# Kernel optimization log

Measured on AMD Instinct MI355X. Metric: run time of the kernel, lower is better.

## Reference

```python
import jax, jax.numpy as jnp
import numpy as np

WS = 3          # windows_size
ND = 3          # num_dilation, dilations [1,2,3]
NSTATE = 16     # d_state
RANK = 12       # dt_rank = ceil(192/16)
TOPK = 36       # max(1,(20//3)**2)*depth
DM = 192        # d_model
DI = 384        # d_inner = 2*d_model
B0, HH, WW = 8, 96, 96


def setup_inputs() -> dict:
    ks = jax.random.split(jax.random.key(0), 12)
    f = jax.random.normal
    return {
        "x": f(ks[0], (B0, HH, WW, DM), jnp.float32),
        "W_in": f(ks[1], (2 * DI, DM), jnp.float32) * 0.02,
        "conv_w": f(ks[2], (DI, 1, 7, 7), jnp.float32) * 0.05,
        "conv_b": f(ks[3], (DI,), jnp.float32) * 0.01,
        "x_proj_w": f(ks[4], (2, RANK + 2 * NSTATE, DI), jnp.float32) * 0.02,
        "dt_w": f(ks[5], (2, DI, RANK), jnp.float32) * 0.02,
        "dt_b": f(ks[6], (2, DI), jnp.float32) * 0.01,
        "A_logs": jnp.tile(jnp.log(jnp.arange(1, NSTATE + 1, dtype=jnp.float32)), (2 * DI, 1)),
        "Ds": jnp.ones((2 * DI,), jnp.float32),
        "W_kv": f(ks[7], (2 * DI, DI), jnp.float32) * 0.02,
        "b_kv": jnp.zeros((2 * DI,), jnp.float32),
        "ln_g": jnp.ones((DI,), jnp.float32),
        "ln_b": jnp.zeros((DI,), jnp.float32),
        "W_out": f(ks[8], (DM, DI), jnp.float32) * 0.02,
    }


def _selective_scan(xs, x_proj_w, dt_w, dt_b, A_logs, Ds):
    # xs: (B, K=2, D, L) -> (B, K, D, L). Standard Mamba selective scan.
    B, K, D, L = xs.shape
    x_dbl = jnp.einsum('bkdl,kcd->bkcl', xs, x_proj_w)          # (B,K,R+2N,L)
    dts = x_dbl[:, :, :RANK]
    Bs = x_dbl[:, :, RANK:RANK + NSTATE]                        # (B,K,N,L)
    Cs = x_dbl[:, :, RANK + NSTATE:]                            # (B,K,N,L)
    delta = jax.nn.softplus(jnp.einsum('bkrl,kdr->bkdl', dts, dt_w) + dt_b[None, :, :, None])
    A = -jnp.exp(A_logs).reshape(K, D, NSTATE)
    dA = jnp.exp(delta[..., None] * A[None, :, :, None, :])    # (B,K,D,L,N)
    dBu = delta[..., None] * Bs.transpose(0, 1, 3, 2)[:, :, None, :, :] * xs[..., None]
    dA = jnp.moveaxis(dA, 3, 0)                                 # (L,B,K,D,N)
    dBu = jnp.moveaxis(dBu, 3, 0)
    C = jnp.moveaxis(Cs, 3, 0)                                  # (L,B,K,N)

    def step(h, inp):
        dA_t, dBu_t, C_t = inp
        h = dA_t * h + dBu_t
        y = jnp.einsum('bkdn,bkn->bkd', h, C_t)
        return h, y

    h0 = jnp.zeros((B, K, D, NSTATE), xs.dtype)
    _, ys = jax.lax.scan(step, h0, (dA, dBu, C))                # ys: (L,B,K,D)
    y = jnp.moveaxis(ys, 0, 3)                                  # (B,K,D,L)
    return y + Ds.reshape(1, K, D, 1) * xs


def _dynamic_mask_active(x):
    # x: (B,D,H,W). Partition into WSxWS windows, keep TOPK by mean activation.
    B, D, H, W = x.shape
    nH, nW = H // WS, W // WS
    w = x.reshape(B, D, nH, WS, nW, WS).transpose(0, 2, 4, 1, 3, 5)
    w = w.reshape(B, nH * nW, D, WS * WS)                       # (B,nWin,D,ws2)
    score = w.mean(axis=(2, 3))                                 # (B,nWin)
    _, idx = jax.lax.top_k(score, TOPK)                         # (B,TOPK)
    g = jnp.take_along_axis(w, idx[:, :, None, None], axis=1)   # (B,TOPK,D,ws2)
    return g.transpose(0, 2, 1, 3).reshape(B, D, TOPK * WS * WS)


def _unfold(x, d):
    # torch nn.Unfold(kernel=WS, dilation=d, padding=d, stride=1) on (B,C,H,W)
    B, C, H, W = x.shape
    xp = jnp.pad(x, ((0, 0), (0, 0), (d, d), (d, d)))
    pats = [xp[:, :, i * d:i * d + H, j * d:j * d + W] for i in range(WS) for j in range(WS)]
    p = jnp.stack(pats, axis=2)                                 # (B,C,ws2,H,W) channel-major like torch
    return p.reshape(B, C, WS * WS, H * W)


def _forward(x, W_in, conv_w, conv_b, x_proj_w, dt_w, dt_b, A_logs, Ds,
             W_kv, b_kv, ln_g, ln_b, W_out):
    B, H, W_, _ = x.shape
    xz = jnp.einsum('bhwc,oc->bhwo', x, W_in)
    xf, z = jnp.split(xz, 2, axis=-1)                           # (B,H,W,DI) each
    xc = xf.transpose(0, 3, 1, 2)
    xc = jax.lax.conv_general_dilated(xc, conv_w, (1, 1), [(3, 3), (3, 3)],
                                      feature_group_count=conv_w.shape[0],
                                      dimension_numbers=('NCHW', 'OIHW', 'NCHW'))
    xc = xc + conv_b[None, :, None, None]                       # (B,DI,H,W)
    D = xc.shape[1]

    # foreground SSM on active windows (forward + flipped scan)
    act = _dynamic_mask_active(xc)                              # (B,D,L)
    xs = jnp.stack([act, jnp.flip(act, axis=-1)], axis=1)       # (B,2,D,L)
    out = _selective_scan(xs, x_proj_w, dt_w, dt_b, A_logs, Ds)
    y1 = out[:, 0] + jnp.flip(out[:, 1], axis=-1)               # (B,D,L)
    y1 = y1.transpose(0, 2, 1)                                  # (B,L,D)

    L = y1.shape[1]
    ws2 = WS * WS
    n2 = L // ws2
    kv = jnp.einsum('bld,od->blo', y1, W_kv) + b_kv             # (B,L,2D)
    hd = 2 * D // ND
    t = kv.reshape(B, n2, ws2, ND, hd).transpose(3, 0, 4, 2, 1)  # (ND,B,hd,ws2,n2)
    Q, Kt = t[:, :, :hd // 2], t[:, :, hd // 2:]                 # (ND,B,D/ND,ws2,n2)

    dch = D // ND
    xr = xc.reshape(B, ND, dch, H, W_)
    ys = []
    for i in range(ND):
        V = _unfold(xr[:, i], i + 1)                            # (B,dch,ws2,n1)
        V = V.transpose(0, 1, 3, 2)                             # (B,dch,n1,ws2)
        s = jnp.einsum('bcwn,bcwn->bcw', Q[i], Kt[i]) / np.sqrt(dch).astype(np.float32)
        # softmax over a singleton axis (as in the source) -> all ones
        A_M = jax.nn.softmax(s[..., None], axis=-1)[..., 0]     # (B,dch,ws2)
        ys.append(jnp.einsum('bcnw,bcw->bcn', V, A_M))          # (B,dch,n1)
    y = jnp.concatenate(ys, axis=1)                             # (B,D,n1)
    y = y.transpose(0, 2, 1)                                    # (B,n1,D)

    mu = y.mean(-1, keepdims=True)
    var = y.var(-1, keepdims=True)
    y = (y - mu) / jnp.sqrt(var + 1e-5) * ln_g + ln_b
    y = y.reshape(B, H, W_, D) + z
    return jnp.einsum('bhwd,od->bhwo', y, W_out)


def reference(x, W_in, conv_w, conv_b, x_proj_w, dt_w, dt_b, A_logs, Ds,
              W_kv, b_kv, ln_g, ln_b, W_out):
    return _forward(x, W_in, conv_w, conv_b, x_proj_w, dt_w, dt_b, A_logs, Ds,
                    W_kv, b_kv, ln_g, ln_b, W_out)
```

## Files before the change

kernel.cpp:

```cpp
#include <hip/hip_runtime.h>
#include <cstddef>

#define B0V 8
#define HSV 96
#define WSV 96
#define DMV 192
#define DIV 384
#define MTOT (B0V*HSV*WSV)

typedef __attribute__((ext_vector_type(8))) unsigned short ushort8v;
typedef __attribute__((ext_vector_type(8))) short short8v;
typedef __attribute__((ext_vector_type(4))) float f32x4;
typedef _Float16 h2 __attribute__((ext_vector_type(2)));
typedef _Float16 h8 __attribute__((ext_vector_type(8)));

__device__ __forceinline__ unsigned short f2bf(float f) {
    unsigned int i; __builtin_memcpy(&i, &f, 4);
    i += 0x7FFFu + ((i >> 16) & 1);
    return (unsigned short)(i >> 16);
}

template<int ROWS>
__device__ __forceinline__ void stageBF16(const unsigned short* __restrict__ src, int ld,
                                          unsigned short* lds, int t) {
#pragma unroll
    for (int i = 0; i < ROWS*8/256; ++i) {
        const int cid = t + i*256;
        const int r = cid >> 3, cb = cid & 7;
        ushort8v sv = *(const ushort8v*)(src + (size_t)r*ld + cb*8);
        *(ushort8v*)((char*)lds + r*128 + ((cb ^ (r&7))<<4)) = sv;
    }
}
__device__ __forceinline__ short8v fragRead(const unsigned short* lds, int row, int kchunk) {
    return *(const short8v*)((const char*)lds + row*128 + ((kchunk ^ (row&7))<<4));
}

__global__ __launch_bounds__(256) void prep_kernel(
    const float* __restrict__ Wout, const float* __restrict__ Win,
    const float* __restrict__ cw,
    unsigned short* __restrict__ Wch, h2* __restrict__ w2h,
    unsigned short* __restrict__ WinfH, unsigned short* __restrict__ WoutH)
{
    const int blk = blockIdx.x;
    const int t = threadIdx.x;
    if (blk < 192) {
        __shared__ float wrow[384];
        for (int j = t; j < 384; j += 256) wrow[j] = Wout[(size_t)blk*384 + j];
        __syncthreads();
        if (t < 192) {
            float acc = 0.f;
#pragma unroll 4
            for (int j = 0; j < 384; ++j)
                acc += wrow[j] * Win[(size_t)(384 + j)*192 + t];
            Wch[(size_t)blk*192 + t] = f2bf(acc);
        }
    } else if (blk < 229) {
        const int idx = (blk - 192)*256 + t;
        if (idx < 49*192) {
            const int tap = idx / 192, cp = idx % 192;
            h2 v;
            v[0] = (_Float16)cw[(size_t)(2*cp  )*49 + tap];
            v[1] = (_Float16)cw[(size_t)(2*cp+1)*49 + tap];
            w2h[idx] = v;
        }
    } else if (blk < 265) {
        const int i = (blk - 229)*256 + t;
        if (i < 384*192/8) {
            const float4 f0 = *(const float4*)(Win + (size_t)i*8);
            const float4 f1 = *(const float4*)(Win + (size_t)i*8 + 4);
            ushort8v v;
            v[0]=f2bf(f0.x); v[1]=f2bf(f0.y); v[2]=f2bf(f0.z); v[3]=f2bf(f0.w);
            v[4]=f2bf(f1.x); v[5]=f2bf(f1.y); v[6]=f2bf(f1.z); v[7]=f2bf(f1.w);
            *(ushort8v*)(WinfH + (size_t)i*8) = v;
        }
    } else {
        const int i = (blk - 265)*256 + t;
        if (i < 192*384/8) {
            const float4 f0 = *(const float4*)(Wout + (size_t)i*8);
            const float4 f1 = *(const float4*)(Wout + (size_t)i*8 + 4);
            ushort8v v;
            v[0]=f2bf(f0.x); v[1]=f2bf(f0.y); v[2]=f2bf(f0.z); v[3]=f2bf(f0.w);
            v[4]=f2bf(f1.x); v[5]=f2bf(f1.y); v[6]=f2bf(f1.z); v[7]=f2bf(f1.w);
            *(ushort8v*)(WoutH + (size_t)i*8) = v;
        }
    }
}

__global__ __launch_bounds__(256) void gemm_in_mfma(
    const float* __restrict__ x, const unsigned short* __restrict__ Wh,
    unsigned short* __restrict__ xh, _Float16* __restrict__ xf)
{
    __shared__ unsigned short As[3*64*64];
    __shared__ unsigned short Bs[128*64];
    const int t = threadIdx.x;
    const int m0 = blockIdx.x * 64;
    const int wid = t >> 6, lane = t & 63;
    const int li = lane & 15, lg = lane >> 4;

#pragma unroll
    for (int kb = 0; kb < 3; ++kb) {
#pragma unroll
        for (int i = 0; i < 2; ++i) {
            const int cid = t + i*256;
            const int r = cid >> 3, cb = cid & 7;
            const float* p = x + (size_t)(m0 + r)*DMV + kb*64 + cb*8;
            float4 f0 = *(const float4*)p;
            float4 f1 = *(const float4*)(p+4);
            ushort8v sv;
            sv[0]=f2bf(f0.x); sv[1]=f2bf(f0.y); sv[2]=f2bf(f0.z); sv[3]=f2bf(f0.w);
            sv[4]=f2bf(f1.x); sv[5]=f2bf(f1.y); sv[6]=f2bf(f1.z); sv[7]=f2bf(f1.w);
            *(ushort8v*)((char*)(As + kb*64*64) + r*128 + ((cb ^ (r&7))<<4)) = sv;
            *(ushort8v*)(xh + (size_t)(m0 + r)*DMV + kb*64 + cb*8) = sv;
        }
    }

    for (int n0i = 0; n0i < 3; ++n0i) {
        const int n0 = n0i * 128;
        f32x4 acc[4][2];
#pragma unroll
        for (int i = 0; i < 4; ++i)
#pragma unroll
            for (int j = 0; j < 2; ++j) acc[i][j] = (f32x4){0.f,0.f,0.f,0.f};

        for (int kb = 0; kb < 3; ++kb) {
            __syncthreads();
            stageBF16<128>(Wh + (size_t)n0*DMV + kb*64, DMV, Bs, t);
            __syncthreads();
#pragma unroll
            for (int ks = 0; ks < 2; ++ks) {
                short8v a[4], b[2];
#pragma unroll
                for (int mf = 0; mf < 4; ++mf)
                    a[mf] = fragRead(As + kb*64*64, mf*16 + li, ks*4 + lg);
#pragma unroll
                for (int nf = 0; nf < 2; ++nf)
                    b[nf] = fragRead(Bs, wid*32 + nf*16 + li, ks*4 + lg);
#pragma unroll
                for (int mf = 0; mf < 4; ++mf)
#pragma unroll
                    for (int nf = 0; nf < 2; ++nf)
                        acc[mf][nf] = __builtin_amdgcn_mfma_f32_16x16x32_bf16(a[mf], b[nf], acc[mf][nf], 0, 0, 0);
            }
        }
#pragma unroll
        for (int mf = 0; mf < 4; ++mf)
#pragma unroll
            for (int nf = 0; nf < 2; ++nf)
#pragma unroll
                for (int i = 0; i < 4; ++i) {
                    const int row = m0 + mf*16 + lg*4 + i;
                    const int col = n0 + wid*32 + nf*16 + li;
                    xf[(size_t)row*DIV + col] = (_Float16)acc[mf][nf][i];
                }
    }
}

__global__ __launch_bounds__(256) void dwconv_kernel(
    const _Float16* __restrict__ xf, const h2* __restrict__ w2h,
    const float* __restrict__ cb, _Float16* __restrict__ xc)
{
    const int id  = blockIdx.x;
    const int swz = (id & 7) * 432 + (id >> 3);
    const int b    = swz / 432;
    const int rem  = swz - b*432;
    const int cg   = rem / 72;
    const int tile = rem - cg*72;
    const int th = tile / 6, tw = tile % 6;
    const int h0 = th*8, w0 = tw*16;
    const int c0 = cg*64;

    __shared__ _Float16 patch[14*22*64];
    const int t = threadIdx.x;
    for (int idx = t; idx < 308*8; idx += 256) {
        const int sp = idx >> 3, c8 = idx & 7;
        const int ih = sp / 22, iw = sp - ih*22;
        const int gh = h0 - 3 + ih, gw = w0 - 3 + iw;
        ushort8v v;
#pragma unroll
        for (int j = 0; j < 8; ++j) v[j] = 0;
        if ((unsigned)gh < (unsigned)HSV && (unsigned)gw < (unsigned)WSV)
            v = *(const ushort8v*)(xf + (((size_t)b*HSV + gh)*WSV + gw)*DIV + c0 + c8*8);
        *(ushort8v*)(patch + sp*64 + c8*8) = v;
    }
    __syncthreads();

    const int cp = t & 31;
    const int wq = t >> 5;

    h2 wreg[49];
    const h2* wp = w2h + (c0 >> 1) + cp;
#pragma unroll
    for (int k = 0; k < 49; ++k) wreg[k] = wp[k*192];

    h2 biasv;
    biasv[0] = (_Float16)cb[c0 + 2*cp];
    biasv[1] = (_Float16)cb[c0 + 2*cp + 1];
    h2 acc[8][2];
#pragma unroll
    for (int i = 0; i < 8; ++i) { acc[i][0] = biasv; acc[i][1] = biasv; }

    const h2* prow = (const h2*)patch;
#pragma unroll
    for (int ih = 0; ih < 14; ++ih) {
        h2 r[8];
#pragma unroll
        for (int j = 0; j < 8; ++j)
            r[j] = prow[(ih*22 + wq*2 + j)*32 + cp];
#pragma unroll
        for (int kw = 0; kw < 7; ++kw) {
#pragma unroll
            for (int oh = 0; oh < 8; ++oh) {
                const int kh = ih - oh;
                if (kh >= 0 && kh < 7) {
                    acc[oh][0] += wreg[kh*7 + kw] * r[kw];
                    acc[oh][1] += wreg[kh*7 + kw] * r[kw + 1];
                }
            }
        }
    }
    h2* xcp = (h2*)xc;
#pragma unroll
    for (int oh = 0; oh < 8; ++oh)
#pragma unroll
        for (int j = 0; j < 2; ++j)
            xcp[((((size_t)b*HSV + h0+oh)*WSV + (w0 + wq*2 + j))*DIV + c0)/2 + cp] = acc[oh][j];
}

__global__ __launch_bounds__(256) void boxln_kernel(
    const _Float16* __restrict__ xc,
    const float* __restrict__ g, const float* __restrict__ bta,
    unsigned short* __restrict__ yln)
{
    const int wid  = threadIdx.x >> 6;
    const int lane = threadIdx.x & 63;
    const int m = blockIdx.x * 4 + wid;
    const int b  = m / (HSV*WSV);
    const int hw = m % (HSV*WSV);
    const int h = hw / WSV, w = hw % WSV;

    const bool act = lane < 48;
    const int ch = lane * 8;
    const int dd = (ch >> 7) + 1;

    float s[8];
#pragma unroll
    for (int j = 0; j < 8; ++j) s[j] = 0.f;

#pragma unroll
    for (int a = -1; a <= 1; ++a)
#pragma unroll
        for (int bb = -1; bb <= 1; ++bb) {
            const int h2_ = h + a*dd, w2_ = w + bb*dd;
            if (act && (unsigned)h2_ < (unsigned)HSV && (unsigned)w2_ < (unsigned)WSV) {
                h8 v = *(const h8*)(xc + (((size_t)b*HSV + h2_)*WSV + w2_)*DIV + ch);
#pragma unroll
                for (int j = 0; j < 8; ++j) s[j] += (float)v[j];
            }
        }

    float ps = 0.f, ps2 = 0.f;
#pragma unroll
    for (int j = 0; j < 8; ++j) { ps += s[j]; ps2 += s[j]*s[j]; }
#pragma unroll
    for (int off = 32; off > 0; off >>= 1) {
        ps  += __shfl_xor(ps,  off);
        ps2 += __shfl_xor(ps2, off);
    }
    const float mu   = ps * (1.f/384.f);
    const float var  = ps2 * (1.f/384.f) - mu*mu;
    const float rstd = rsqrtf(var + 1e-5f);

    if (act) {
        float4 g0 = *(const float4*)(g + ch);
        float4 g1 = *(const float4*)(g + ch + 4);
        float4 b0 = *(const float4*)(bta + ch);
        float4 b1 = *(const float4*)(bta + ch + 4);
        float gv[8] = {g0.x,g0.y,g0.z,g0.w,g1.x,g1.y,g1.z,g1.w};
        float bv[8] = {b0.x,b0.y,b0.z,b0.w,b1.x,b1.y,b1.z,b1.w};
        ushort8v o;
#pragma unroll
        for (int j = 0; j < 8; ++j)
            o[j] = f2bf((s[j] - mu)*rstd*gv[j] + bv[j]);
        *(ushort8v*)(yln + (size_t)m*DIV + ch) = o;
    }
}

__global__ __launch_bounds__(256) void gemm_out_mfma(
    const unsigned short* __restrict__ Yl, const unsigned short* __restrict__ WoutH,
    const unsigned short* __restrict__ xh, const unsigned short* __restrict__ Wch,
    float* __restrict__ out)
{
    __shared__ unsigned short As[64*64];
    __shared__ unsigned short Bs[192*64];
    const int t = threadIdx.x;
    const int m0 = blockIdx.x * 64;
    const int wid = t >> 6, lane = t & 63;
    const int li = lane & 15, lg = lane >> 4;

    f32x4 acc[4][3];
#pragma unroll
    for (int i = 0; i < 4; ++i)
#pragma unroll
        for (int j = 0; j < 3; ++j) acc[i][j] = (f32x4){0.f,0.f,0.f,0.f};

    for (int kb = 0; kb < 9; ++kb) {
        if (kb < 6) {
            stageBF16<64> (Yl + (size_t)m0*DIV + kb*64, DIV, As, t);
            stageBF16<192>(WoutH + kb*64, DIV, Bs, t);
        } else {
            stageBF16<64> (xh + (size_t)m0*DMV + (kb-6)*64, DMV, As, t);
            stageBF16<192>(Wch + (kb-6)*64, DMV, Bs, t);
        }
        __syncthreads();
#pragma unroll
        for (int ks = 0; ks < 2; ++ks) {
            short8v a[4], b[3];
#pragma unroll
            for (int mf = 0; mf < 4; ++mf) a[mf] = fragRead(As, mf*16 + li, ks*4 + lg);
#pragma unroll
            for (int nf = 0; nf < 3; ++nf) b[nf] = fragRead(Bs, wid*48 + nf*16 + li, ks*4 + lg);
#pragma unroll
            for (int mf = 0; mf < 4; ++mf)
#pragma unroll
                for (int nf = 0; nf < 3; ++nf)
                    acc[mf][nf] = __builtin_amdgcn_mfma_f32_16x16x32_bf16(a[mf], b[nf], acc[mf][nf], 0, 0, 0);
        }
        __syncthreads();
    }
#pragma unroll
    for (int mf = 0; mf < 4; ++mf)
#pragma unroll
        for (int nf = 0; nf < 3; ++nf)
#pragma unroll
            for (int i = 0; i < 4; ++i) {
                const int row = m0 + mf*16 + lg*4 + i;
                const int col = wid*48 + nf*16 + li;
                out[(size_t)row*DMV + col] = acc[mf][nf][i];
            }
}

extern "C" void kernel_launch(void* const* d_in, const int* in_sizes, int n_in,
                              void* d_out, int out_size, void* d_ws, size_t ws_size,
                              hipStream_t stream)
{
    const float* x      = (const float*)d_in[0];
    const float* W_in   = (const float*)d_in[1];
    const float* conv_w = (const float*)d_in[2];
    const float* conv_b = (const float*)d_in[3];
    const float* ln_g   = (const float*)d_in[11];
    const float* ln_b   = (const float*)d_in[12];
    const float* W_out  = (const float*)d_in[13];
    float* out = (float*)d_out;

    char* ws = (char*)d_ws;
    unsigned short* Wch   = (unsigned short*)(ws);
    h2*             w2h   = (h2*)(ws + 0x20000);
    unsigned short* WinfH = (unsigned short*)(ws + 0x40000);
    unsigned short* WoutH = (unsigned short*)(ws + 0x80000);
    unsigned short* xh    = (unsigned short*)(ws + 0x100000);
    _Float16*       xf    = (_Float16*)(ws + 0x2000000);
    _Float16*       xc    = (_Float16*)d_out;

    prep_kernel  <<<dim3(301),          256, 0, stream>>>(W_out, W_in, conv_w,
                                                          Wch, w2h, WinfH, WoutH);
    gemm_in_mfma <<<dim3(MTOT/64),      256, 0, stream>>>(x, WinfH, xh, xf);
    dwconv_kernel<<<dim3(3456),         256, 0, stream>>>(xf, w2h, conv_b, xc);
    boxln_kernel <<<dim3(MTOT/4),       256, 0, stream>>>(xc, ln_g, ln_b,
                                                          (unsigned short*)xf);
    gemm_out_mfma<<<dim3(MTOT/64),      256, 0, stream>>>((const unsigned short*)xf,
                                                          WoutH, xh, Wch, out);
}
```

Before: 206.9 us.

## Fuse box-sum layernorm into output GEMM via shared-memory A tiles

The box-filter plus layernorm stage is merged into the output GEMM kernel. Each block computes the normalized bf16 rows for its 64 pixels straight into a 48KB swizzled LDS buffer, so the yln intermediate no longer makes a global round trip and one launch is dropped. Buffer roles are swapped so the conv output lives in the workspace while d_out holds xf, since out is now written while xc is still being read. The larger LDS allocation may lower occupancy, and the LN phase is serialized before the MFMA loop inside each block.

```diff
diff --git a/kernel.cpp b/kernel.cpp
--- a/kernel.cpp
+++ b/kernel.cpp
@@ -226,77 +226,80 @@
             xcp[((((size_t)b*HSV + h0+oh)*WSV + (w0 + wq*2 + j))*DIV + c0)/2 + cp] = acc[oh][j];
 }
 
-__global__ __launch_bounds__(256) void boxln_kernel(
+__global__ __launch_bounds__(256) void fused_ln_gemm_out(
     const _Float16* __restrict__ xc,
     const float* __restrict__ g, const float* __restrict__ bta,
-    unsigned short* __restrict__ yln)
-{
-    const int wid  = threadIdx.x >> 6;
-    const int lane = threadIdx.x & 63;
-    const int m = blockIdx.x * 4 + wid;
-    const int b  = m / (HSV*WSV);
-    const int hw = m % (HSV*WSV);
-    const int h = hw / WSV, w = hw % WSV;
-
-    const bool act = lane < 48;
-    const int ch = lane * 8;
-    const int dd = (ch >> 7) + 1;
-
-    float s[8];
-#pragma unroll
-    for (int j = 0; j < 8; ++j) s[j] = 0.f;
-
-#pragma unroll
-    for (int a = -1; a <= 1; ++a)
-#pragma unroll
-        for (int bb = -1; bb <= 1; ++bb) {
-            const int h2_ = h + a*dd, w2_ = w + bb*dd;
-            if (act && (unsigned)h2_ < (unsigned)HSV && (unsigned)w2_ < (unsigned)WSV) {
-                h8 v = *(const h8*)(xc + (((size_t)b*HSV + h2_)*WSV + w2_)*DIV + ch);
-#pragma unroll
-                for (int j = 0; j < 8; ++j) s[j] += (float)v[j];
-            }
-        }
-
-    float ps = 0.f, ps2 = 0.f;
-#pragma unroll
-    for (int j = 0; j < 8; ++j) { ps += s[j]; ps2 += s[j]*s[j]; }
-#pragma unroll
-    for (int off = 32; off > 0; off >>= 1) {
-        ps  += __shfl_xor(ps,  off);
-        ps2 += __shfl_xor(ps2, off);
-    }
-    const float mu   = ps * (1.f/384.f);
-    const float var  = ps2 * (1.f/384.f) - mu*mu;
-    const float rstd = rsqrtf(var + 1e-5f);
-
-    if (act) {
-        float4 g0 = *(const float4*)(g + ch);
-        float4 g1 = *(const float4*)(g + ch + 4);
-        float4 b0 = *(const float4*)(bta + ch);
-        float4 b1 = *(const float4*)(bta + ch + 4);
-        float gv[8] = {g0.x,g0.y,g0.z,g0.w,g1.x,g1.y,g1.z,g1.w};
-        float bv[8] = {b0.x,b0.y,b0.z,b0.w,b1.x,b1.y,b1.z,b1.w};
-        ushort8v o;
-#pragma unroll
-        for (int j = 0; j < 8; ++j)
-            o[j] = f2bf((s[j] - mu)*rstd*gv[j] + bv[j]);
-        *(ushort8v*)(yln + (size_t)m*DIV + ch) = o;
-    }
-}
-
-__global__ __launch_bounds__(256) void gemm_out_mfma(
-    const unsigned short* __restrict__ Yl, const unsigned short* __restrict__ WoutH,
+    const unsigned short* __restrict__ WoutH,
     const unsigned short* __restrict__ xh, const unsigned short* __restrict__ Wch,
     float* __restrict__ out)
 {
-    __shared__ unsigned short As[64*64];
+    __shared__ unsigned short As[6*64*64];
     __shared__ unsigned short Bs[192*64];
     const int t = threadIdx.x;
     const int m0 = blockIdx.x * 64;
     const int wid = t >> 6, lane = t & 63;
     const int li = lane & 15, lg = lane >> 4;
 
+    {
+        const bool act = lane < 48;
+        const int ch = lane * 8;
+        const int dd = (ch >> 7) + 1;
+        const int kbA = lane >> 3;
+        const int cb  = lane & 7;
+        float gv[8], bv[8];
+        if (act) {
+            float4 g0 = *(const float4*)(g + ch);
+            float4 g1 = *(const float4*)(g + ch + 4);
+            float4 b0 = *(const float4*)(bta + ch);
+            float4 b1 = *(const float4*)(bta + ch + 4);
+            gv[0]=g0.x; gv[1]=g0.y; gv[2]=g0.z; gv[3]=g0.w;
+            gv[4]=g1.x; gv[5]=g1.y; gv[6]=g1.z; gv[7]=g1.w;
+            bv[0]=b0.x; bv[1]=b0.y; bv[2]=b0.z; bv[3]=b0.w;
+            bv[4]=b1.x; bv[5]=b1.y; bv[6]=b1.z; bv[7]=b1.w;
+        }
+        for (int it = 0; it < 16; ++it) {
+            const int pl = it*4 + wid;
+            const int m = m0 + pl;
+            const int b  = m / (HSV*WSV);
+            const int hw = m % (HSV*WSV);
+            const int h = hw / WSV, w = hw % WSV;
+
+            float s[8];
+#pragma unroll
+            for (int j = 0; j < 8; ++j) s[j] = 0.f;
+#pragma unroll
+            for (int a = -1; a <= 1; ++a)
+#pragma unroll
+                for (int bb = -1; bb <= 1; ++bb) {
+                    const int h2_ = h + a*dd, w2_ = w + bb*dd;
+                    if (act && (unsigned)h2_ < (unsigned)HSV && (unsigned)w2_ < (unsigned)WSV) {
+                        h8 v = *(const h8*)(xc + (((size_t)b*HSV + h2_)*WSV + w2_)*DIV + ch);
+#pragma unroll
+                        for (int j = 0; j < 8; ++j) s[j] += (float)v[j];
+                    }
+                }
+            float ps = 0.f, ps2 = 0.f;
+#pragma unroll
+            for (int j = 0; j < 8; ++j) { ps += s[j]; ps2 += s[j]*s[j]; }
+#pragma unroll
+            for (int off = 32; off > 0; off >>= 1) {
+                ps  += __shfl_xor(ps,  off);
+                ps2 += __shfl_xor(ps2, off);
+            }
+            const float mu   = ps * (1.f/384.f);
+            const float var  = ps2 * (1.f/384.f) - mu*mu;
+            const float rstd = rsqrtf(var + 1e-5f);
+            if (act) {
+                ushort8v o;
+#pragma unroll
+                for (int j = 0; j < 8; ++j)
+                    o[j] = f2bf((s[j] - mu)*rstd*gv[j] + bv[j]);
+                *(ushort8v*)((char*)(As + kbA*64*64) + pl*128 + ((cb ^ (pl&7))<<4)) = o;
+            }
+        }
+    }
+    __syncthreads();
+
     f32x4 acc[4][3];
 #pragma unroll
     for (int i = 0; i < 4; ++i)
@@ -304,19 +307,21 @@
         for (int j = 0; j < 3; ++j) acc[i][j] = (f32x4){0.f,0.f,0.f,0.f};
 
     for (int kb = 0; kb < 9; ++kb) {
+        const unsigned short* Acur;
         if (kb < 6) {
-            stageBF16<64> (Yl + (size_t)m0*DIV + kb*64, DIV, As, t);
             stageBF16<192>(WoutH + kb*64, DIV, Bs, t);
+            Acur = As + kb*64*64;
         } else {
-            stageBF16<64> (xh + (size_t)m0*DMV + (kb-6)*64, DMV, As, t);
+            stageBF16<64> (xh + (size_t)m0*DMV + (kb-6)*64, DMV, As + (kb-6)*64*64, t);
             stageBF16<192>(Wch + (kb-6)*64, DMV, Bs, t);
+            Acur = As + (kb-6)*64*64;
         }
         __syncthreads();
 #pragma unroll
         for (int ks = 0; ks < 2; ++ks) {
             short8v a[4], b[3];
 #pragma unroll
-            for (int mf = 0; mf < 4; ++mf) a[mf] = fragRead(As, mf*16 + li, ks*4 + lg);
+            for (int mf = 0; mf < 4; ++mf) a[mf] = fragRead(Acur, mf*16 + li, ks*4 + lg);
 #pragma unroll
             for (int nf = 0; nf < 3; ++nf) b[nf] = fragRead(Bs, wid*48 + nf*16 + li, ks*4 + lg);
 #pragma unroll
@@ -358,15 +363,13 @@
     unsigned short* WinfH = (unsigned short*)(ws + 0x40000);
     unsigned short* WoutH = (unsigned short*)(ws + 0x80000);
     unsigned short* xh    = (unsigned short*)(ws + 0x100000);
-    _Float16*       xf    = (_Float16*)(ws + 0x2000000);
-    _Float16*       xc    = (_Float16*)d_out;
-
-    prep_kernel  <<<dim3(301),          256, 0, stream>>>(W_out, W_in, conv_w,
-                                                          Wch, w2h, WinfH, WoutH);
-    gemm_in_mfma <<<dim3(MTOT/64),      256, 0, stream>>>(x, WinfH, xh, xf);
-    dwconv_kernel<<<dim3(3456),         256, 0, stream>>>(xf, w2h, conv_b, xc);
-    boxln_kernel <<<dim3(MTOT/4),       256, 0, stream>>>(xc, ln_g, ln_b,
-                                                          (unsigned short*)xf);
-    gemm_out_mfma<<<dim3(MTOT/64),      256, 0, stream>>>((const unsigned short*)xf,
-                                                          WoutH, xh, Wch, out);
-}
+    _Float16*       xc    = (_Float16*)(ws + 0x2000000);
+    _Float16*       xf    = (_Float16*)d_out;
+
+    prep_kernel     <<<dim3(301),      256, 0, stream>>>(W_out, W_in, conv_w,
+                                                         Wch, w2h, WinfH, WoutH);
+    gemm_in_mfma    <<<dim3(MTOT/64),  256, 0, stream>>>(x, WinfH, xh, xf);
+    dwconv_kernel   <<<dim3(3456),     256, 0, stream>>>(xf, w2h, conv_b, xc);
+    fused_ln_gemm_out<<<dim3(MTOT/64), 256, 0, stream>>>(xc, ln_g, ln_b,
+                                                         WoutH, xh, Wch, out);
+}
```

After: 284.6 us. 1.38x slower.
